# Kernel optimization log

Measured on AMD Instinct MI355X. Metric: run time of the kernel, lower is better.

The kernel has to match this reference:

```python
import jax, jax.numpy as jnp
import numpy as np

B, S, N_NODES, D_IN = 8, 24, 400, 3
D_MODEL = 32
G1_HEADS, G1_DIM = 4, 16
G2_HEADS, G2_DIM = 1, 32
T_KEY = 32


def _ln(x, g, b, eps=1e-6):
    m = jnp.mean(x, -1, keepdims=True)
    v = jnp.var(x, -1, keepdims=True)
    return g * (x - m) / jnp.sqrt(v + eps) + b


def _gat(x, adj, wq, bq, wk, bk, wv, bv, heads, dim):
    # x: [B*, N, F]; adjacency-masked multi-head attention (GraphAttention)
    Bx, N, _ = x.shape
    q = (x @ wq + bq).reshape(Bx, N, heads, dim)
    k = (x @ wk + bk).reshape(Bx, N, heads, dim)
    v = (x @ wv + bv).reshape(Bx, N, heads, dim)
    s = jnp.einsum('bihd,bjhd->bhij', q, k) / jnp.sqrt(jnp.float32(dim))
    s = jnp.where((adj == 0)[None, None], jnp.float32(-1e9), s)
    w = jax.nn.softmax(s, axis=-1)
    o = jnp.einsum('bhij,bjhd->bihd', w, v)
    return o.reshape(Bx, N, heads * dim)


def _mha(x, wq, bq, wk, bk, wv, bv, wo, bo):
    # keras MultiHeadAttention(num_heads=2, key_dim=32), self-attention, output dim = 32
    q = jnp.einsum('bsd,dhk->bshk', x, wq) + bq
    k = jnp.einsum('bsd,dhk->bshk', x, wk) + bk
    v = jnp.einsum('bsd,dhk->bshk', x, wv) + bv
    a = jax.nn.softmax(jnp.einsum('bqhk,bshk->bhqs', q, k) / jnp.sqrt(jnp.float32(T_KEY)), axis=-1)
    o = jnp.einsum('bhqs,bshk->bqhk', a, v)
    return jnp.einsum('bqhk,hko->bqo', o, wo) + bo


def setup_inputs() -> dict:
    ks = jax.random.split(jax.random.key(0), 20)

    def w(k, shape, scale=0.05):
        return (jax.random.normal(k, shape) * scale).astype(jnp.float32)

    z = lambda *s: jnp.zeros(s, jnp.float32)
    one = lambda *s: jnp.ones(s, jnp.float32)

    d = {}
    d['inputs'] = jax.random.normal(ks[0], (B, S, N_NODES, D_IN), dtype=jnp.float32)
    adj = (jax.random.uniform(ks[1], (N_NODES, N_NODES)) < 0.05).astype(jnp.float32)
    adj = jnp.minimum(adj + jnp.eye(N_NODES, dtype=jnp.float32), 1.0)
    d['adj'] = adj / (jnp.sum(adj, axis=1, keepdims=True) + 1e-6)  # row-normalized

    d['g1_wq'] = w(ks[2], (D_IN, G1_HEADS * G1_DIM)); d['g1_bq'] = z(G1_HEADS * G1_DIM)
    d['g1_wk'] = w(ks[3], (D_IN, G1_HEADS * G1_DIM)); d['g1_bk'] = z(G1_HEADS * G1_DIM)
    d['g1_wv'] = w(ks[4], (D_IN, G1_HEADS * G1_DIM)); d['g1_bv'] = z(G1_HEADS * G1_DIM)
    d['g2_wq'] = w(ks[5], (G1_HEADS * G1_DIM, G2_DIM)); d['g2_bq'] = z(G2_DIM)
    d['g2_wk'] = w(ks[6], (G1_HEADS * G1_DIM, G2_DIM)); d['g2_bk'] = z(G2_DIM)
    d['g2_wv'] = w(ks[7], (G1_HEADS * G1_DIM, G2_DIM)); d['g2_bv'] = z(G2_DIM)
    d['sp_g'] = one(D_MODEL); d['sp_b'] = z(D_MODEL)
    d['t_wq'] = w(ks[8], (D_MODEL, 2, T_KEY)); d['t_bq'] = z(2, T_KEY)
    d['t_wk'] = w(ks[9], (D_MODEL, 2, T_KEY)); d['t_bk'] = z(2, T_KEY)
    d['t_wv'] = w(ks[10], (D_MODEL, 2, T_KEY)); d['t_bv'] = z(2, T_KEY)
    d['t_wo'] = w(ks[11], (2, T_KEY, D_MODEL)); d['t_bo'] = z(D_MODEL)
    d['ff_w1'] = w(ks[12], (D_MODEL, 64)); d['ff_b1'] = z(64)
    d['ff_w2'] = w(ks[13], (64, D_MODEL)); d['ff_b2'] = z(D_MODEL)
    d['ln1_g'] = one(D_MODEL); d['ln1_b'] = z(D_MODEL)
    d['ln2_g'] = one(D_MODEL); d['ln2_b'] = z(D_MODEL)
    d['fin_g'] = one(D_MODEL); d['fin_b'] = z(D_MODEL)
    d['fd_w'] = w(ks[14], (D_MODEL, 1), scale=0.01); d['fd_b'] = z(1)
    return d


def reference(inputs, adj, g1_wq, g1_bq, g1_wk, g1_bk, g1_wv, g1_bv,
              g2_wq, g2_bq, g2_wk, g2_bk, g2_wv, g2_bv, sp_g, sp_b,
              t_wq, t_bq, t_wk, t_bk, t_wv, t_bv, t_wo, t_bo,
              ff_w1, ff_b1, ff_w2, ff_b2, ln1_g, ln1_b, ln2_g, ln2_b,
              fin_g, fin_b, fd_w, fd_b):
    Bx, Sx, N, _ = inputs.shape
    x = inputs.reshape(Bx * Sx, N, D_IN)

    # SpatialProcessor: GAT1 -> relu -> GAT2 -> residual layernorm
    h = jax.nn.relu(_gat(x, adj, g1_wq, g1_bq, g1_wk, g1_bk, g1_wv, g1_bv, G1_HEADS, G1_DIM))
    h = _gat(h, adj, g2_wq, g2_bq, g2_wk, g2_bk, g2_wv, g2_bv, G2_HEADS, G2_DIM)
    res = jnp.pad(x, ((0, 0), (0, 0), (0, D_MODEL - D_IN)))  # zero-pad 3 -> 32 for residual
    sp = _ln(h + res, sp_g, sp_b)
    sp4 = sp.reshape(Bx, Sx, N, D_MODEL)  # [B, S, N, 32]

    # TemporalTransformer over sequence per node
    t_in = jnp.transpose(sp4, (0, 2, 1, 3)).reshape(Bx * N, Sx, D_MODEL)
    a = _mha(t_in, t_wq, t_bq, t_wk, t_bk, t_wv, t_bv, t_wo, t_bo)
    x1 = _ln(t_in + a, ln1_g, ln1_b)
    f = jax.nn.gelu(x1 @ ff_w1 + ff_b1, approximate=False) @ ff_w2 + ff_b2
    t_out = _ln(x1 + f, ln2_g, ln2_b).reshape(Bx, N, Sx, D_MODEL)

    # fuse: mean over seq (spatial) + mean over seq (temporal), layernorm, final dense
    fused = _ln(jnp.mean(sp4, axis=1) + jnp.mean(t_out, axis=2), fin_g, fin_b)
    return (fused @ fd_w + fd_b)[..., 0]  # [B, N]
```

## Files before the change

### kernel.cpp

```cpp
#include <hip/hip_runtime.h>
#include <hip/hip_bf16.h>

#define NN 400
#define KMAX 64

struct WTab {
  const void* p[34];
  int off[35];
};

__device__ __forceinline__ float bflo(unsigned u) {
  union { unsigned i; float f; } x; x.i = u << 16; return x.f;
}
__device__ __forceinline__ float bfhi(unsigned u) {
  union { unsigned i; float f; } x; x.i = u & 0xffff0000u; return x.f;
}
__device__ __forceinline__ unsigned short f2bf(float f) {
  __hip_bfloat16 b = __float2bfloat16(f);
  return *reinterpret_cast<unsigned short*>(&b);
}
__device__ __forceinline__ unsigned packbf(float a, float b) {
  return (unsigned)f2bf(a) | ((unsigned)f2bf(b) << 16);
}
__device__ __forceinline__ bool detect_bf16(const unsigned short* probe) {
  int lane = threadIdx.x & 63;
  unsigned short u = probe[lane * 2];
  int e = (u >> 7) & 0xFF;
  bool plaus = (u == 0) || (e >= 112 && e <= 132);
  return __popcll(__ballot(plaus)) >= 48;
}
__device__ __forceinline__ float rsum32(float v) {
  v += __shfl_xor(v, 1); v += __shfl_xor(v, 2); v += __shfl_xor(v, 4);
  v += __shfl_xor(v, 8); v += __shfl_xor(v, 16); return v;
}

__global__ __launch_bounds__(256) void prep_k(
    WTab wt, const void* __restrict__ adj,
    const unsigned short* __restrict__ probe, float* __restrict__ dst,
    int* __restrict__ colp, int* __restrict__ degp) {
  bool isbf = detect_bf16(probe);
  const int tid = threadIdx.x;
  if (blockIdx.x < 40) {
    int total = wt.off[34];
    for (int i = blockIdx.x * 256 + tid; i < total; i += 40 * 256) {
      int lo = 0, hi = 33;
      while (lo < hi) {
        int mid = (lo + hi + 1) >> 1;
        if (i >= wt.off[mid]) lo = mid; else hi = mid - 1;
      }
      int rel = i - wt.off[lo];
      float v;
      if (isbf) v = __bfloat162float(((const __hip_bfloat16*)wt.p[lo])[rel]);
      else      v = ((const float*)wt.p[lo])[rel];
      dst[i] = v;
    }
  } else {
    int row = (blockIdx.x - 40) * 4 + (tid >> 6);
    int lane = tid & 63;
    int base = 0;
    for (int j0 = 0; j0 < NN; j0 += 64) {
      int j = j0 + lane;
      bool nz;
      if (isbf) nz = (j < NN) && ((const unsigned short*)adj)[row * NN + j] != 0;
      else      nz = (j < NN) && ((const float*)adj)[row * NN + j] != 0.0f;
      unsigned long long m = __ballot(nz);
      int offl = __popcll(m & ((1ull << lane) - 1ull));
      if (nz) {
        int pidx = base + offl;
        if (pidx < KMAX) colp[row * KMAX + pidx] = j;
      }
      base += __popcll(m);
    }
    if (lane == 0) degp[row] = base < KMAX ? base : KMAX;
  }
}

__global__ __launch_bounds__(256) void gat1_k(
    const void* __restrict__ xraw, const unsigned short* __restrict__ probe,
    const float* __restrict__ g1, const int* __restrict__ colp,
    const int* __restrict__ degp, unsigned short* __restrict__ h1b) {
  __shared__ float xsf[NN * 4];
  __shared__ float yhf[4 * NN * 4];
  __shared__ float w1s[768];
  __shared__ float cf[64];
  const int tid = threadIdx.x;
  const int g = blockIdx.x;
  bool isbf = detect_bf16(probe);

  for (int e = tid; e < 768; e += 256) w1s[e] = g1[e];
  for (int e = tid; e < NN; e += 256) xsf[e * 4 + 3] = 0.f;
  for (int e = tid; e < NN * 3; e += 256) {
    int j = e / 3, a = e - j * 3;
    float v;
    if (isbf) v = __bfloat162float(((const __hip_bfloat16*)xraw)[g * NN * 3 + e]);
    else      v = ((const float*)xraw)[g * NN * 3 + e];
    xsf[j * 4 + a] = v;
  }
  __syncthreads();

  if (tid < 64) {
    int h = tid >> 4, t = tid & 15, co = h * 16;
    float acc = 0.f;
    if (t < 9) {
      int a = t / 3, b = t - (t / 3) * 3;
      for (int c = 0; c < 16; ++c) acc += w1s[a * 64 + co + c] * w1s[256 + b * 64 + co + c];
    } else if (t < 12) {
      int a = t - 9;
      for (int c = 0; c < 16; ++c) acc += w1s[a * 64 + co + c] * w1s[448 + co + c];
    } else if (t < 15) {
      int b = t - 12;
      for (int c = 0; c < 16; ++c) acc += w1s[256 + b * 64 + co + c] * w1s[192 + co + c];
    } else {
      for (int c = 0; c < 16; ++c) acc += w1s[192 + co + c] * w1s[448 + co + c];
    }
    cf[h * 16 + t] = acc;
  }
  __syncthreads();

  for (int e = tid; e < NN * 4; e += 256) {
    int j = e >> 2, h = e & 3;
    const float* bse = cf + h * 16;
    float x0 = xsf[j * 4], x1 = xsf[j * 4 + 1], x2 = xsf[j * 4 + 2];
    float* y = yhf + (h * NN + j) * 4;
    y[0] = bse[0] * x0 + bse[1] * x1 + bse[2] * x2;
    y[1] = bse[3] * x0 + bse[4] * x1 + bse[5] * x2;
    y[2] = bse[6] * x0 + bse[7] * x1 + bse[8] * x2;
    y[3] = bse[12] * x0 + bse[13] * x1 + bse[14] * x2 + bse[15];
  }
  __syncthreads();

  const float4* xs4 = (const float4*)xsf;
  const float4* yh4 = (const float4*)yhf;
  const int i0 = blockIdx.y * 200;
  for (int i = i0 + tid; i < i0 + 200; i += 256) {
    float4 xi = xs4[i];
    float ch[4];
    #pragma unroll
    for (int h = 0; h < 4; ++h)
      ch[h] = cf[h * 16 + 9] * xi.x + cf[h * 16 + 10] * xi.y + cf[h * 16 + 11] * xi.z;
    float l[4] = {0.f, 0.f, 0.f, 0.f};
    float ax[4], ay[4], az[4];
    #pragma unroll
    for (int h = 0; h < 4; ++h) { ax[h] = 0.f; ay[h] = 0.f; az[h] = 0.f; }
    int dg = degp[i];
    const int* cols = colp + i * KMAX;
    for (int e = 0; e < dg; ++e) {
      int j = cols[e];
      float4 xj = xs4[j];
      #pragma unroll
      for (int h = 0; h < 4; ++h) {
        float4 y = yh4[h * NN + j];
        float s = (xi.x * y.x + xi.y * y.y + xi.z * y.z + y.w + ch[h]) * 0.25f;
        float p = __expf(s);
        l[h] += p;
        ax[h] += p * xj.x; ay[h] += p * xj.y; az[h] += p * xj.z;
      }
    }
    unsigned* hr = (unsigned*)(h1b + ((size_t)g * NN + i) * 64);
    #pragma unroll
    for (int h = 0; h < 4; ++h) {
      float inv = 1.f / l[h];
      float b0 = ax[h] * inv, b1 = ay[h] * inv, b2 = az[h] * inv;
      int co = h * 16;
      #pragma unroll
      for (int c = 0; c < 16; c += 2) {
        float o0 = fmaxf(b0 * w1s[512 + co + c] + b1 * w1s[576 + co + c] +
                         b2 * w1s[640 + co + c] + w1s[704 + co + c], 0.f);
        float o1 = fmaxf(b0 * w1s[513 + co + c] + b1 * w1s[577 + co + c] +
                         b2 * w1s[641 + co + c] + w1s[705 + co + c], 0.f);
        hr[(co + c) >> 1] = packbf(o0, o1);
      }
    }
  }
}

__global__ __launch_bounds__(256) void gat2_proj_k(
    const unsigned short* __restrict__ h1b, const float* __restrict__ g2,
    unsigned short* __restrict__ q2b, unsigned short* __restrict__ k2g,
    unsigned short* __restrict__ v2g) {
  __shared__ float ht[64 * 68];
  const int tid = threadIdx.x, t = blockIdx.x;
  for (int e = tid; e < 2048; e += 256) {
    unsigned u = ((const unsigned*)h1b)[t * 2048 + e];
    int ln = e >> 5, d0 = (e & 31) * 2;
    ht[d0 * 68 + ln] = bflo(u);
    ht[(d0 + 1) * 68 + ln] = bfhi(u);
  }
  __syncthreads();
  const int c = tid & 31, ng = tid >> 5;
  const float* wq = g2;
  const float* wk = g2 + 2080;
  const float* wv = g2 + 4160;
  float qa[8], ka[8], va[8];
  float bq = g2[2048 + c], bk = g2[4128 + c], bv = g2[6208 + c];
  #pragma unroll
  for (int k = 0; k < 8; ++k) { qa[k] = bq; ka[k] = bk; va[k] = bv; }
  for (int d = 0; d < 64; ++d) {
    float wqv = wq[d * 32 + c], wkv = wk[d * 32 + c], wvv = wv[d * 32 + c];
    const float4* hp = (const float4*)(ht + d * 68 + ng * 8);
    float4 h0 = hp[0], h1v = hp[1];
    float hv[8] = {h0.x, h0.y, h0.z, h0.w, h1v.x, h1v.y, h1v.z, h1v.w};
    #pragma unroll
    for (int k = 0; k < 8; ++k) {
      qa[k] += hv[k] * wqv; ka[k] += hv[k] * wkv; va[k] += hv[k] * wvv;
    }
  }
  #pragma unroll
  for (int k = 0; k < 8; ++k) {
    int gn = t * 64 + ng * 8 + k;
    q2b[gn * 32 + c] = f2bf(qa[k]);
    k2g[gn * 32 + c] = f2bf(ka[k]);
    v2g[gn * 32 + c] = f2bf(va[k]);
  }
}

__global__ __launch_bounds__(256) void gat2_attn_k(
    const void* __restrict__ xraw, const unsigned short* __restrict__ probe,
    const unsigned short* __restrict__ q2b, const unsigned short* __restrict__ k2g,
    const unsigned short* __restrict__ v2g, const float* __restrict__ spw,
    const int* __restrict__ colp, const int* __restrict__ degp,
    float* __restrict__ spo) {
  __shared__ unsigned short k2s[NN * 40];
  __shared__ unsigned short v2s[NN * 40];
  __shared__ float gw[64];
  const int tid = threadIdx.x;
  const int g = blockIdx.x;
  bool isbf = detect_bf16(probe);
  if (tid < 64) gw[tid] = spw[tid];
  for (int e = tid; e < 3200; e += 256) {
    uint2 uk = ((const uint2*)k2g)[g * 3200 + e];
    uint2 uv = ((const uint2*)v2g)[g * 3200 + e];
    int n = e >> 3, c = (e & 7) * 2;
    *(uint2*)((unsigned*)k2s + n * 20 + c) = uk;
    *(uint2*)((unsigned*)v2s + n * 20 + c) = uv;
  }
  __syncthreads();
  const int b = g / 24, st = g % 24;
  const int i0 = blockIdx.y * 100;
  for (int i = i0 + tid; i < i0 + 100; i += 256) {
    const uint4* qp = (const uint4*)(q2b + ((size_t)g * NN + i) * 32);
    uint4 qw[4] = {qp[0], qp[1], qp[2], qp[3]};
    float q[32], o[32];
    #pragma unroll
    for (int t = 0; t < 4; ++t) {
      unsigned uu[4] = {qw[t].x, qw[t].y, qw[t].z, qw[t].w};
      #pragma unroll
      for (int m = 0; m < 4; ++m) {
        q[t * 8 + 2 * m] = bflo(uu[m]); q[t * 8 + 2 * m + 1] = bfhi(uu[m]);
      }
    }
    #pragma unroll
    for (int c = 0; c < 32; ++c) o[c] = 0.f;
    int dg = degp[i];
    const int* cols = colp + i * KMAX;
    float l = 0.f;
    for (int e = 0; e < dg; ++e) {
      int j = cols[e];
      const uint4* kr = (const uint4*)(k2s + j * 40);
      const uint4* vr = (const uint4*)(v2s + j * 40);
      float s = 0.f;
      #pragma unroll
      for (int t = 0; t < 4; ++t) {
        uint4 kk = kr[t];
        unsigned uu[4] = {kk.x, kk.y, kk.z, kk.w};
        #pragma unroll
        for (int m = 0; m < 4; ++m)
          s += q[t * 8 + 2 * m] * bflo(uu[m]) + q[t * 8 + 2 * m + 1] * bfhi(uu[m]);
      }
      float p = __expf(s * 0.17677669529663688f);
      l += p;
      #pragma unroll
      for (int t = 0; t < 4; ++t) {
        uint4 vv = vr[t];
        unsigned uu[4] = {vv.x, vv.y, vv.z, vv.w};
        #pragma unroll
        for (int m = 0; m < 4; ++m) {
          o[t * 8 + 2 * m]     += p * bflo(uu[m]);
          o[t * 8 + 2 * m + 1] += p * bfhi(uu[m]);
        }
      }
    }
    float inv = 1.f / l;
    float xr[3];
    #pragma unroll
    for (int a = 0; a < 3; ++a) {
      if (isbf) xr[a] = __bfloat162float(((const __hip_bfloat16*)xraw)[((size_t)g * NN + i) * 3 + a]);
      else      xr[a] = ((const float*)xraw)[((size_t)g * NN + i) * 3 + a];
    }
    float row[32];
    #pragma unroll
    for (int c = 0; c < 32; ++c) row[c] = o[c] * inv;
    row[0] += xr[0]; row[1] += xr[1]; row[2] += xr[2];
    float mean = 0.f;
    #pragma unroll
    for (int c = 0; c < 32; ++c) mean += row[c];
    mean *= (1.f / 32.f);
    float var = 0.f;
    #pragma unroll
    for (int c = 0; c < 32; ++c) { float dd = row[c] - mean; var += dd * dd; }
    var *= (1.f / 32.f);
    float rinv = 1.f / sqrtf(var + 1e-6f);
    float4* so4 = (float4*)(spo + (((size_t)b * NN + i) * 24 + st) * 32);
    #pragma unroll
    for (int k = 0; k < 8; ++k) {
      float4 v;
      v.x = gw[4 * k]     * (row[4 * k]     - mean) * rinv + gw[32 + 4 * k];
      v.y = gw[4 * k + 1] * (row[4 * k + 1] - mean) * rinv + gw[33 + 4 * k];
      v.z = gw[4 * k + 2] * (row[4 * k + 2] - mean) * rinv + gw[34 + 4 * k];
      v.w = gw[4 * k + 3] * (row[4 * k + 3] - mean) * rinv + gw[35 + 4 * k];
      so4[k] = v;
    }
  }
}

__global__ __launch_bounds__(128) void temporal_k(
    const float* __restrict__ sp, const float* __restrict__ tw,
    const unsigned short* __restrict__ probe, void* __restrict__ outp) {
  __shared__ float sm[6648];
  float* t_s = sm;
  float* q_s = sm + 768;
  float* k_s = sm + 2328;
  float* v_s = sm + 3888;
  float* aw  = sm + 5448;
  float* x1s = sm + 5448;
  float* att = q_s;
  float* f1s = k_s;
  float* tos = v_s;
  const int tid = threadIdx.x;
  bool isbf = detect_bf16(probe);

  const float* twq = tw;            const float* tbq = tw + 2048;
  const float* twk = tw + 2112;     const float* tbk = tw + 4160;
  const float* twv = tw + 4224;     const float* tbv = tw + 6272;
  const float* two = tw + 6336;     const float* tbo = tw + 8384;
  const float* fw1 = tw + 8416;     const float* fb1 = tw + 10464;
  const float* fw2 = tw + 10528;    const float* fb2 = tw + 12576;
  const float* l1g = tw + 12608;    const float* l1b = tw + 12640;
  const float* l2g = tw + 12672;    const float* l2b = tw + 12704;
  const float* fng = tw + 12736;    const float* fnb = tw + 12768;
  const float* fdw = tw + 12800;    const float* fdb = tw + 12832;

  const float4* base4 = (const float4*)(sp + (size_t)blockIdx.x * 768);
  for (int e = tid; e < 192; e += 128) ((float4*)t_s)[e] = base4[e];
  __syncthreads();

  {
    const int hk = tid & 63, sh = tid >> 6;
    for (int a = 0; a < 3; ++a) {
      const float* W  = (a == 0) ? twq : (a == 1) ? twk : twv;
      const float* Bb = (a == 0) ? tbq : (a == 1) ? tbk : tbv;
      float* dst      = (a == 0) ? q_s : (a == 1) ? k_s : v_s;
      float w[32];
      #pragma unroll
      for (int c = 0; c < 32; ++c) w[c] = W[c * 64 + hk];
      float bias = Bb[hk];
      for (int s = sh * 12; s < sh * 12 + 12; ++s) {
        float acc = bias;
        const float* tr = t_s + s * 32;
        #pragma unroll
        for (int c = 0; c < 32; ++c) acc += tr[c] * w[c];
        dst[s * 65 + hk] = acc;
      }
    }
  }
  __syncthreads();

  if (tid < 96) {
    const int h = tid / 48, rem = tid % 48, qs = rem >> 1, half = rem & 1;
    const float* qr = q_s + qs * 65 + h * 32;
    float sc[12], l = 0.f;
    #pragma unroll
    for (int k = 0; k < 12; ++k) {
      const float* kr = k_s + (half * 12 + k) * 65 + h * 32;
      float s = 0.f;
      #pragma unroll
      for (int d = 0; d < 32; ++d) s += qr[d] * kr[d];
      sc[k] = __expf(s * 0.17677669529663688f);
      l += sc[k];
    }
    l += __shfl_xor(l, 1);
    float inv = 1.f / l;
    float* ar = aw + (h * 24 + qs) * 25 + half * 12;
    #pragma unroll
    for (int k = 0; k < 12; ++k) ar[k] = sc[k] * inv;
  }
  __syncthreads();

  for (int e = tid; e < 1536; e += 128) {
    int qs = e >> 6, hk = e & 63, h = hk >> 5;
    const float* ar = aw + (h * 24 + qs) * 25;
    float a = 0.f;
    #pragma unroll
    for (int ss = 0; ss < 24; ++ss) a += ar[ss] * v_s[ss * 65 + hk];
    att[qs * 65 + hk] = a;
  }
  __syncthreads();

  for (int e = tid; e < 768; e += 128) {
    int s = e >> 5, c = e & 31;
    const float* ar = att + s * 65;
    float a = tbo[c];
    #pragma unroll 8
    for (int hk = 0; hk < 64; ++hk) a += ar[hk] * two[hk * 32 + c];
    x1s[s * 33 + c] = t_s[e] + a;
  }
  __syncthreads();
  if (tid < 24) {
    float* r = x1s + tid * 33;
    float mean = 0.f;
    for (int c = 0; c < 32; ++c) mean += r[c];
    mean *= (1.f / 32.f);
    float var = 0.f;
    for (int c = 0; c < 32; ++c) { float d = r[c] - mean; var += d * d; }
    var *= (1.f / 32.f);
    float ri = 1.f / sqrtf(var + 1e-6f);
    for (int c = 0; c < 32; ++c) r[c] = l1g[c] * (r[c] - mean) * ri + l1b[c];
  }
  __syncthreads();

  {
    const int j = tid & 63, sh = tid >> 6;
    float w[32];
    #pragma unroll
    for (int c = 0; c < 32; ++c) w[c] = fw1[c * 64 + j];
    float bias = fb1[j];
    for (int s = sh * 12; s < sh * 12 + 12; ++s) {
      float acc = bias;
      const float* xr = x1s + s * 33;
      #pragma unroll
      for (int c = 0; c < 32; ++c) acc += xr[c] * w[c];
      f1s[s * 64 + j] = 0.5f * acc * (1.f + erff(acc * 0.70710678118654752f));
    }
  }
  __syncthreads();

  for (int e = tid; e < 768; e += 128) {
    int s = e >> 5, c = e & 31;
    const float* fr = f1s + s * 64;
    float a = fb2[c];
    #pragma unroll 8
    for (int j = 0; j < 64; ++j) a += fr[j] * fw2[j * 32 + c];
    tos[s * 33 + c] = x1s[s * 33 + c] + a;
  }
  __syncthreads();
  if (tid < 24) {
    float* r = tos + tid * 33;
    float mean = 0.f;
    for (int c = 0; c < 32; ++c) mean += r[c];
    mean *= (1.f / 32.f);
    float var = 0.f;
    for (int c = 0; c < 32; ++c) { float d = r[c] - mean; var += d * d; }
    var *= (1.f / 32.f);
    float ri = 1.f / sqrtf(var + 1e-6f);
    for (int c = 0; c < 32; ++c) r[c] = l2g[c] * (r[c] - mean) * ri + l2b[c];
  }
  __syncthreads();

  if (tid < 32) {
    const int c = tid;
    float ms = 0.f, mt = 0.f;
    #pragma unroll
    for (int s = 0; s < 24; ++s) { ms += t_s[s * 32 + c]; mt += tos[s * 33 + c]; }
    float red = (ms + mt) * (1.f / 24.f);
    float mean = rsum32(red) * (1.f / 32.f);
    float dv = red - mean;
    float var = rsum32(dv * dv) * (1.f / 32.f);
    float ri = 1.f / sqrtf(var + 1e-6f);
    float y = (fng[c] * dv * ri + fnb[c]) * fdw[c];
    float tot = rsum32(y);
    if (c == 0) {
      float acc = tot + fdb[0];
      if (isbf) ((__hip_bfloat16*)outp)[blockIdx.x] = __float2bfloat16(acc);
      else      ((float*)outp)[blockIdx.x] = acc;
    }
  }
}

extern "C" void kernel_launch(void* const* d_in, const int* in_sizes, int n_in,
                              void* d_out, int out_size, void* d_ws, size_t ws_size,
                              hipStream_t stream) {
  static const int wsizes[34] = {
      192, 64, 192, 64, 192, 64,
      2048, 32, 2048, 32, 2048, 32,
      32, 32,
      2048, 64, 2048, 64, 2048, 64, 2048, 32,
      2048, 64, 2048, 32,
      32, 32, 32, 32, 32, 32,
      32, 1};
  WTab wt;
  int off = 0;
  for (int i = 0; i < 34; ++i) { wt.p[i] = d_in[i + 2]; wt.off[i] = off; off += wsizes[i]; }
  wt.off[34] = off;

  char* ws = (char*)d_ws;
  float* convw = (float*)ws;
  int*   colp  = (int*)(ws + 81920);
  int*   degp  = (int*)(ws + 184320);
  unsigned short* h1b = (unsigned short*)(ws + 196608);
  float*          spo = (float*)(ws + 196608);
  unsigned short* q2b = (unsigned short*)(ws + 10027008);
  unsigned short* k2g = (unsigned short*)(ws + 14942208);
  unsigned short* v2g = (unsigned short*)(ws + 19857408);

  const float* g1  = convw;
  const float* g2  = convw + 768;
  const float* spw = convw + 7008;
  const float* twp = convw + 7072;
  const unsigned short* probe = (const unsigned short*)d_in[0];

  hipLaunchKernelGGL(prep_k, dim3(140), dim3(256), 0, stream, wt, d_in[1], probe,
                     convw, colp, degp);
  hipLaunchKernelGGL(gat1_k, dim3(192, 2), dim3(256), 0, stream, d_in[0], probe,
                     g1, (const int*)colp, (const int*)degp, h1b);
  hipLaunchKernelGGL(gat2_proj_k, dim3(1200), dim3(256), 0, stream,
                     (const unsigned short*)h1b, g2, q2b, k2g, v2g);
  hipLaunchKernelGGL(gat2_attn_k, dim3(192, 4), dim3(256), 0, stream, d_in[0],
                     probe, (const unsigned short*)q2b, (const unsigned short*)k2g,
                     (const unsigned short*)v2g, spw, (const int*)colp,
                     (const int*)degp, spo);
  hipLaunchKernelGGL(temporal_k, dim3(3200), dim3(128), 0, stream,
                     (const float*)spo, twp, probe, d_out);
}
```

Before: 319.5 us.

## Fuse GAT2 projection and attention into one kernel with LDS-resident K/V

Merges the GAT2 QKV projection kernel and the attention kernel into a single kernel, one block per graph. Each block projects all 400 nodes in chunks of 64 and writes K and V directly into shared memory, so they never round-trip through global memory. Q still goes through global memory and is re-read by the same block. The K/V row stride becomes 34 shorts to avoid bank conflicts, which also turns the vector loads into dword loads. In exchange, the grid drops from 192x4 blocks to 192 blocks, and each block does its projection chunks and attention rows serially, which reduces parallelism.

```diff
diff --git a/kernel.cpp b/kernel.cpp
--- a/kernel.cpp
+++ b/kernel.cpp
@@ -174,70 +174,65 @@
   }
 }
 
-__global__ __launch_bounds__(256) void gat2_proj_k(
+__global__ __launch_bounds__(256) void projattn_k(
+    const void* __restrict__ xraw, const unsigned short* __restrict__ probe,
     const unsigned short* __restrict__ h1b, const float* __restrict__ g2,
-    unsigned short* __restrict__ q2b, unsigned short* __restrict__ k2g,
-    unsigned short* __restrict__ v2g) {
-  __shared__ float ht[64 * 68];
-  const int tid = threadIdx.x, t = blockIdx.x;
-  for (int e = tid; e < 2048; e += 256) {
-    unsigned u = ((const unsigned*)h1b)[t * 2048 + e];
-    int ln = e >> 5, d0 = (e & 31) * 2;
-    ht[d0 * 68 + ln] = bflo(u);
-    ht[(d0 + 1) * 68 + ln] = bfhi(u);
-  }
-  __syncthreads();
-  const int c = tid & 31, ng = tid >> 5;
-  const float* wq = g2;
-  const float* wk = g2 + 2080;
-  const float* wv = g2 + 4160;
-  float qa[8], ka[8], va[8];
-  float bq = g2[2048 + c], bk = g2[4128 + c], bv = g2[6208 + c];
-  #pragma unroll
-  for (int k = 0; k < 8; ++k) { qa[k] = bq; ka[k] = bk; va[k] = bv; }
-  for (int d = 0; d < 64; ++d) {
-    float wqv = wq[d * 32 + c], wkv = wk[d * 32 + c], wvv = wv[d * 32 + c];
-    const float4* hp = (const float4*)(ht + d * 68 + ng * 8);
-    float4 h0 = hp[0], h1v = hp[1];
-    float hv[8] = {h0.x, h0.y, h0.z, h0.w, h1v.x, h1v.y, h1v.z, h1v.w};
-    #pragma unroll
-    for (int k = 0; k < 8; ++k) {
-      qa[k] += hv[k] * wqv; ka[k] += hv[k] * wkv; va[k] += hv[k] * wvv;
-    }
-  }
-  #pragma unroll
-  for (int k = 0; k < 8; ++k) {
-    int gn = t * 64 + ng * 8 + k;
-    q2b[gn * 32 + c] = f2bf(qa[k]);
-    k2g[gn * 32 + c] = f2bf(ka[k]);
-    v2g[gn * 32 + c] = f2bf(va[k]);
-  }
-}
-
-__global__ __launch_bounds__(256) void gat2_attn_k(
-    const void* __restrict__ xraw, const unsigned short* __restrict__ probe,
-    const unsigned short* __restrict__ q2b, const unsigned short* __restrict__ k2g,
-    const unsigned short* __restrict__ v2g, const float* __restrict__ spw,
-    const int* __restrict__ colp, const int* __restrict__ degp,
+    const float* __restrict__ spw, const int* __restrict__ colp,
+    const int* __restrict__ degp, unsigned short* __restrict__ q2b,
     float* __restrict__ spo) {
-  __shared__ unsigned short k2s[NN * 40];
-  __shared__ unsigned short v2s[NN * 40];
+  __shared__ __align__(16) unsigned short ht[64 * 72];
+  __shared__ unsigned short k2s[NN * 34];
+  __shared__ unsigned short v2s[NN * 34];
   __shared__ float gw[64];
   const int tid = threadIdx.x;
   const int g = blockIdx.x;
   bool isbf = detect_bf16(probe);
   if (tid < 64) gw[tid] = spw[tid];
-  for (int e = tid; e < 3200; e += 256) {
-    uint2 uk = ((const uint2*)k2g)[g * 3200 + e];
-    uint2 uv = ((const uint2*)v2g)[g * 3200 + e];
-    int n = e >> 3, c = (e & 7) * 2;
-    *(uint2*)((unsigned*)k2s + n * 20 + c) = uk;
-    *(uint2*)((unsigned*)v2s + n * 20 + c) = uv;
-  }
-  __syncthreads();
+
+  for (int c0 = 0; c0 < NN; c0 += 64) {
+    const int rem = (NN - c0) < 64 ? (NN - c0) : 64;
+    for (int e = tid; e < rem * 32; e += 256) {
+      int ln = e >> 5, dp = e & 31;
+      unsigned u = ((const unsigned*)h1b)[((size_t)g * NN + c0 + ln) * 32 + dp];
+      ht[(2 * dp) * 72 + ln]     = (unsigned short)(u & 0xffffu);
+      ht[(2 * dp + 1) * 72 + ln] = (unsigned short)(u >> 16);
+    }
+    __syncthreads();
+    const int c = tid & 31, ng = tid >> 5;
+    const int nbase = ng * 8;
+    if (nbase < rem) {
+      const float* wq = g2;
+      const float* wk = g2 + 2080;
+      const float* wv = g2 + 4160;
+      float qa[8], ka[8], va[8];
+      float bq = g2[2048 + c], bk = g2[4128 + c], bv = g2[6208 + c];
+      #pragma unroll
+      for (int k = 0; k < 8; ++k) { qa[k] = bq; ka[k] = bk; va[k] = bv; }
+      for (int d = 0; d < 64; ++d) {
+        float wqv = wq[d * 32 + c], wkv = wk[d * 32 + c], wvv = wv[d * 32 + c];
+        uint4 hv4 = *(const uint4*)(ht + d * 72 + nbase);
+        unsigned uu[4] = {hv4.x, hv4.y, hv4.z, hv4.w};
+        #pragma unroll
+        for (int m = 0; m < 4; ++m) {
+          float h0 = bflo(uu[m]), h1v = bfhi(uu[m]);
+          qa[2*m] += h0 * wqv;   qa[2*m+1] += h1v * wqv;
+          ka[2*m] += h0 * wkv;   ka[2*m+1] += h1v * wkv;
+          va[2*m] += h0 * wvv;   va[2*m+1] += h1v * wvv;
+        }
+      }
+      #pragma unroll
+      for (int k = 0; k < 8; ++k) {
+        int n = c0 + nbase + k;
+        q2b[((size_t)g * NN + n) * 32 + c] = f2bf(qa[k]);
+        k2s[n * 34 + c] = f2bf(ka[k]);
+        v2s[n * 34 + c] = f2bf(va[k]);
+      }
+    }
+    __syncthreads();
+  }
+
   const int b = g / 24, st = g % 24;
-  const int i0 = blockIdx.y * 100;
-  for (int i = i0 + tid; i < i0 + 100; i += 256) {
+  for (int i = tid; i < NN; i += 256) {
     const uint4* qp = (const uint4*)(q2b + ((size_t)g * NN + i) * 32);
     uint4 qw[4] = {qp[0], qp[1], qp[2], qp[3]};
     float q[32], o[32];
@@ -256,28 +251,21 @@
     float l = 0.f;
     for (int e = 0; e < dg; ++e) {
       int j = cols[e];
-      const uint4* kr = (const uint4*)(k2s + j * 40);
-      const uint4* vr = (const uint4*)(v2s + j * 40);
+      const unsigned* kr = (const unsigned*)(k2s + j * 34);
       float s = 0.f;
       #pragma unroll
-      for (int t = 0; t < 4; ++t) {
-        uint4 kk = kr[t];
-        unsigned uu[4] = {kk.x, kk.y, kk.z, kk.w};
-        #pragma unroll
-        for (int m = 0; m < 4; ++m)
-          s += q[t * 8 + 2 * m] * bflo(uu[m]) + q[t * 8 + 2 * m + 1] * bfhi(uu[m]);
+      for (int m = 0; m < 16; ++m) {
+        unsigned u = kr[m];
+        s += q[2 * m] * bflo(u) + q[2 * m + 1] * bfhi(u);
       }
       float p = __expf(s * 0.17677669529663688f);
       l += p;
-      #pragma unroll
-      for (int t = 0; t < 4; ++t) {
-        uint4 vv = vr[t];
-        unsigned uu[4] = {vv.x, vv.y, vv.z, vv.w};
-        #pragma unroll
-        for (int m = 0; m < 4; ++m) {
-          o[t * 8 + 2 * m]     += p * bflo(uu[m]);
-          o[t * 8 + 2 * m + 1] += p * bfhi(uu[m]);
-        }
+      const unsigned* vr = (const unsigned*)(v2s + j * 34);
+      #pragma unroll
+      for (int m = 0; m < 16; ++m) {
+        unsigned u = vr[m];
+        o[2 * m]     += p * bflo(u);
+        o[2 * m + 1] += p * bfhi(u);
       }
     }
     float inv = 1.f / l;
@@ -497,10 +485,8 @@
   int*   colp  = (int*)(ws + 81920);
   int*   degp  = (int*)(ws + 184320);
   unsigned short* h1b = (unsigned short*)(ws + 196608);
-  float*          spo = (float*)(ws + 196608);
   unsigned short* q2b = (unsigned short*)(ws + 10027008);
-  unsigned short* k2g = (unsigned short*)(ws + 14942208);
-  unsigned short* v2g = (unsigned short*)(ws + 19857408);
+  float*          spo = (float*)(ws + 14942208);
 
   const float* g1  = convw;
   const float* g2  = convw + 768;
@@ -512,12 +498,9 @@
                      convw, colp, degp);
   hipLaunchKernelGGL(gat1_k, dim3(192, 2), dim3(256), 0, stream, d_in[0], probe,
                      g1, (const int*)colp, (const int*)degp, h1b);
-  hipLaunchKernelGGL(gat2_proj_k, dim3(1200), dim3(256), 0, stream,
-                     (const unsigned short*)h1b, g2, q2b, k2g, v2g);
-  hipLaunchKernelGGL(gat2_attn_k, dim3(192, 4), dim3(256), 0, stream, d_in[0],
-                     probe, (const unsigned short*)q2b, (const unsigned short*)k2g,
-                     (const unsigned short*)v2g, spw, (const int*)colp,
-                     (const int*)degp, spo);
+  hipLaunchKernelGGL(projattn_k, dim3(192), dim3(256), 0, stream, d_in[0], probe,
+                     (const unsigned short*)h1b, g2, spw, (const int*)colp,
+                     (const int*)degp, q2b, spo);
   hipLaunchKernelGGL(temporal_k, dim3(3200), dim3(128), 0, stream,
                      (const float*)spo, twp, probe, d_out);
 }
```

Measured after the change: 346.1 us. 8.3% more time.

## Fuse GAT1 output with GAT2 QKV projection and widen attention row tiles

Applied to the files above, without the earlier changes.

Merges the GAT1 attention kernel and the GAT2 q/k/v projection kernel into one. The ReLU'd GAT1 features are now staged in shared memory as bf16 instead of being written to and reread from global memory, which removes the intermediate h1 buffer and one launch. The workspace layout is compacted to match. The GAT2 attention grid also shrinks from four to two row blocks per graph, so each block covers 200 rows. In exchange, per-block shared memory grows and fewer blocks run in the attention stage.

```diff
diff --git a/kernel.cpp b/kernel.cpp
--- a/kernel.cpp
+++ b/kernel.cpp
@@ -75,16 +75,21 @@
   }
 }
 
-__global__ __launch_bounds__(256) void gat1_k(
+__global__ __launch_bounds__(256) void gat1proj_k(
     const void* __restrict__ xraw, const unsigned short* __restrict__ probe,
-    const float* __restrict__ g1, const int* __restrict__ colp,
-    const int* __restrict__ degp, unsigned short* __restrict__ h1b) {
-  __shared__ float xsf[NN * 4];
-  __shared__ float yhf[4 * NN * 4];
-  __shared__ float w1s[768];
-  __shared__ float cf[64];
+    const float* __restrict__ g1, const float* __restrict__ g2,
+    const int* __restrict__ colp, const int* __restrict__ degp,
+    unsigned short* __restrict__ q2b, unsigned short* __restrict__ k2g,
+    unsigned short* __restrict__ v2g) {
+  __shared__ __align__(16) float smf[8832];
+  float* xsf = smf;
+  float* yhf = smf + 1600;
+  float* w1s = smf + 8000;
+  float* cf  = smf + 8768;
+  unsigned short* ht = (unsigned short*)smf;
   const int tid = threadIdx.x;
   const int g = blockIdx.x;
+  const int i0 = blockIdx.y * 200;
   bool isbf = detect_bf16(probe);
 
   for (int e = tid; e < 768; e += 256) w1s[e] = g1[e];
@@ -131,17 +136,18 @@
 
   const float4* xs4 = (const float4*)xsf;
   const float4* yh4 = (const float4*)yhf;
-  const int i0 = blockIdx.y * 200;
-  for (int i = i0 + tid; i < i0 + 200; i += 256) {
+  float bx[4], by[4], bz[4];
+  const bool act = tid < 200;
+  const int i = i0 + tid;
+  if (act) {
     float4 xi = xs4[i];
     float ch[4];
     #pragma unroll
     for (int h = 0; h < 4; ++h)
       ch[h] = cf[h * 16 + 9] * xi.x + cf[h * 16 + 10] * xi.y + cf[h * 16 + 11] * xi.z;
     float l[4] = {0.f, 0.f, 0.f, 0.f};
-    float ax[4], ay[4], az[4];
-    #pragma unroll
-    for (int h = 0; h < 4; ++h) { ax[h] = 0.f; ay[h] = 0.f; az[h] = 0.f; }
+    #pragma unroll
+    for (int h = 0; h < 4; ++h) { bx[h] = 0.f; by[h] = 0.f; bz[h] = 0.f; }
     int dg = degp[i];
     const int* cols = colp + i * KMAX;
     for (int e = 0; e < dg; ++e) {
@@ -153,64 +159,65 @@
         float s = (xi.x * y.x + xi.y * y.y + xi.z * y.z + y.w + ch[h]) * 0.25f;
         float p = __expf(s);
         l[h] += p;
-        ax[h] += p * xj.x; ay[h] += p * xj.y; az[h] += p * xj.z;
-      }
-    }
-    unsigned* hr = (unsigned*)(h1b + ((size_t)g * NN + i) * 64);
+        bx[h] += p * xj.x; by[h] += p * xj.y; bz[h] += p * xj.z;
+      }
+    }
     #pragma unroll
     for (int h = 0; h < 4; ++h) {
       float inv = 1.f / l[h];
-      float b0 = ax[h] * inv, b1 = ay[h] * inv, b2 = az[h] * inv;
+      bx[h] *= inv; by[h] *= inv; bz[h] *= inv;
+    }
+  }
+  __syncthreads();
+
+  if (act) {
+    #pragma unroll
+    for (int h = 0; h < 4; ++h) {
       int co = h * 16;
       #pragma unroll
-      for (int c = 0; c < 16; c += 2) {
-        float o0 = fmaxf(b0 * w1s[512 + co + c] + b1 * w1s[576 + co + c] +
-                         b2 * w1s[640 + co + c] + w1s[704 + co + c], 0.f);
-        float o1 = fmaxf(b0 * w1s[513 + co + c] + b1 * w1s[577 + co + c] +
-                         b2 * w1s[641 + co + c] + w1s[705 + co + c], 0.f);
-        hr[(co + c) >> 1] = packbf(o0, o1);
-      }
-    }
-  }
-}
-
-__global__ __launch_bounds__(256) void gat2_proj_k(
-    const unsigned short* __restrict__ h1b, const float* __restrict__ g2,
-    unsigned short* __restrict__ q2b, unsigned short* __restrict__ k2g,
-    unsigned short* __restrict__ v2g) {
-  __shared__ float ht[64 * 68];
-  const int tid = threadIdx.x, t = blockIdx.x;
-  for (int e = tid; e < 2048; e += 256) {
-    unsigned u = ((const unsigned*)h1b)[t * 2048 + e];
-    int ln = e >> 5, d0 = (e & 31) * 2;
-    ht[d0 * 68 + ln] = bflo(u);
-    ht[(d0 + 1) * 68 + ln] = bfhi(u);
-  }
-  __syncthreads();
-  const int c = tid & 31, ng = tid >> 5;
-  const float* wq = g2;
-  const float* wk = g2 + 2080;
-  const float* wv = g2 + 4160;
-  float qa[8], ka[8], va[8];
-  float bq = g2[2048 + c], bk = g2[4128 + c], bv = g2[6208 + c];
-  #pragma unroll
-  for (int k = 0; k < 8; ++k) { qa[k] = bq; ka[k] = bk; va[k] = bv; }
-  for (int d = 0; d < 64; ++d) {
-    float wqv = wq[d * 32 + c], wkv = wk[d * 32 + c], wvv = wv[d * 32 + c];
-    const float4* hp = (const float4*)(ht + d * 68 + ng * 8);
-    float4 h0 = hp[0], h1v = hp[1];
-    float hv[8] = {h0.x, h0.y, h0.z, h0.w, h1v.x, h1v.y, h1v.z, h1v.w};
-    #pragma unroll
-    for (int k = 0; k < 8; ++k) {
-      qa[k] += hv[k] * wqv; ka[k] += hv[k] * wkv; va[k] += hv[k] * wvv;
-    }
-  }
-  #pragma unroll
-  for (int k = 0; k < 8; ++k) {
-    int gn = t * 64 + ng * 8 + k;
-    q2b[gn * 32 + c] = f2bf(qa[k]);
-    k2g[gn * 32 + c] = f2bf(ka[k]);
-    v2g[gn * 32 + c] = f2bf(va[k]);
+      for (int c = 0; c < 16; ++c) {
+        int d = co + c;
+        float hd = fmaxf(bx[h] * w1s[512 + d] + by[h] * w1s[576 + d] +
+                         bz[h] * w1s[640 + d] + w1s[704 + d], 0.f);
+        ht[d * 208 + tid] = f2bf(hd);
+      }
+    }
+  }
+  __syncthreads();
+
+  {
+    const int c = tid & 31, ng = tid >> 5;
+    const float* wq = g2;
+    const float* wk = g2 + 2080;
+    const float* wv = g2 + 4160;
+    const float bq = g2[2048 + c], bk = g2[4128 + c], bv = g2[6208 + c];
+    for (int base = 0; base < 200; base += 64) {
+      const int nb = base + ng * 8;
+      if (nb < 200) {
+        float qa[8], ka[8], va[8];
+        #pragma unroll
+        for (int k = 0; k < 8; ++k) { qa[k] = bq; ka[k] = bk; va[k] = bv; }
+        for (int d = 0; d < 64; ++d) {
+          float wqv = wq[d * 32 + c], wkv = wk[d * 32 + c], wvv = wv[d * 32 + c];
+          uint4 hv4 = *(const uint4*)(ht + d * 208 + nb);
+          unsigned uu[4] = {hv4.x, hv4.y, hv4.z, hv4.w};
+          #pragma unroll
+          for (int m = 0; m < 4; ++m) {
+            float h0 = bflo(uu[m]), h1v = bfhi(uu[m]);
+            qa[2*m] += h0 * wqv;   qa[2*m+1] += h1v * wqv;
+            ka[2*m] += h0 * wkv;   ka[2*m+1] += h1v * wkv;
+            va[2*m] += h0 * wvv;   va[2*m+1] += h1v * wvv;
+          }
+        }
+        #pragma unroll
+        for (int k = 0; k < 8; ++k) {
+          size_t gn = (size_t)g * NN + i0 + nb + k;
+          q2b[gn * 32 + c] = f2bf(qa[k]);
+          k2g[gn * 32 + c] = f2bf(ka[k]);
+          v2g[gn * 32 + c] = f2bf(va[k]);
+        }
+      }
+    }
   }
 }
 
@@ -236,8 +243,8 @@
   }
   __syncthreads();
   const int b = g / 24, st = g % 24;
-  const int i0 = blockIdx.y * 100;
-  for (int i = i0 + tid; i < i0 + 100; i += 256) {
+  const int i0 = blockIdx.y * 200;
+  for (int i = i0 + tid; i < i0 + 200; i += 256) {
     const uint4* qp = (const uint4*)(q2b + ((size_t)g * NN + i) * 32);
     uint4 qw[4] = {qp[0], qp[1], qp[2], qp[3]};
     float q[32], o[32];
@@ -496,11 +503,10 @@
   float* convw = (float*)ws;
   int*   colp  = (int*)(ws + 81920);
   int*   degp  = (int*)(ws + 184320);
-  unsigned short* h1b = (unsigned short*)(ws + 196608);
-  float*          spo = (float*)(ws + 196608);
-  unsigned short* q2b = (unsigned short*)(ws + 10027008);
-  unsigned short* k2g = (unsigned short*)(ws + 14942208);
-  unsigned short* v2g = (unsigned short*)(ws + 19857408);
+  unsigned short* q2b = (unsigned short*)(ws + 196608);
+  unsigned short* k2g = (unsigned short*)(ws + 5242880);
+  unsigned short* v2g = (unsigned short*)(ws + 10289152);
+  float*          spo = (float*)(ws + 15335424);
 
   const float* g1  = convw;
   const float* g2  = convw + 768;
@@ -510,11 +516,10 @@
 
   hipLaunchKernelGGL(prep_k, dim3(140), dim3(256), 0, stream, wt, d_in[1], probe,
                      convw, colp, degp);
-  hipLaunchKernelGGL(gat1_k, dim3(192, 2), dim3(256), 0, stream, d_in[0], probe,
-                     g1, (const int*)colp, (const int*)degp, h1b);
-  hipLaunchKernelGGL(gat2_proj_k, dim3(1200), dim3(256), 0, stream,
-                     (const unsigned short*)h1b, g2, q2b, k2g, v2g);
-  hipLaunchKernelGGL(gat2_attn_k, dim3(192, 4), dim3(256), 0, stream, d_in[0],
+  hipLaunchKernelGGL(gat1proj_k, dim3(192, 2), dim3(256), 0, stream, d_in[0],
+                     probe, g1, g2, (const int*)colp, (const int*)degp,
+                     q2b, k2g, v2g);
+  hipLaunchKernelGGL(gat2_attn_k, dim3(192, 2), dim3(256), 0, stream, d_in[0],
                      probe, (const unsigned short*)q2b, (const unsigned short*)k2g,
                      (const unsigned short*)v2g, spw, (const int*)colp,
                      (const int*)degp, spo);
```

Result: faster. 299.8 us (-6.2%).
